# Kernel optimization log

Hardware: AMD Instinct MI355X
Metric: run time of the kernel (lower is better)

The kernel has to match this reference:

```python
import jax, jax.numpy as jnp
import numpy as np

N = 8192       # nodes
F_IN = 512     # input features
H = 8          # heads (layer 1)
C1 = 8         # per-head channels (layer 1)
NC = 16        # num classes
E = 262144     # edges (avg degree 32)
NEG_SLOPE = 0.2


def setup_inputs() -> dict:
    key = jax.random.key(0)
    ks = jax.random.split(key, 11)
    s = 0.1
    return {
        "x": jax.random.normal(ks[0], (N, F_IN), jnp.float32),
        "edge_index": jax.random.randint(ks[1], (2, E), 0, N, dtype=jnp.int32),
        "W1": jax.random.normal(ks[2], (F_IN, H * C1), jnp.float32) * s,
        "a_src1": jax.random.normal(ks[3], (H, C1), jnp.float32) * s,
        "a_dst1": jax.random.normal(ks[4], (H, C1), jnp.float32) * s,
        "b1": jnp.zeros((H * C1,), jnp.float32),
        "W2": jax.random.normal(ks[5], (H * C1, NC), jnp.float32) * s,
        "a_src2": jax.random.normal(ks[6], (1, NC), jnp.float32) * s,
        "a_dst2": jax.random.normal(ks[7], (1, NC), jnp.float32) * s,
        "b2": jnp.zeros((NC,), jnp.float32),
    }


def _gat_layer(x, W, a_src, a_dst, b, src, dst, heads, outc, concat):
    n = x.shape[0]
    h = (x @ W).reshape(n, heads, outc)                      # [N,H,C]
    al_s = jnp.einsum('nhc,hc->nh', h, a_src)                 # [N,H]
    al_d = jnp.einsum('nhc,hc->nh', h, a_dst)                 # [N,H]
    e = jax.nn.leaky_relu(al_s[src] + al_d[dst], NEG_SLOPE)   # [E,H]
    # segment softmax over destination node (every node has a self-loop)
    m = jax.ops.segment_max(e, dst, num_segments=n)
    ex = jnp.exp(e - m[dst])
    denom = jax.ops.segment_sum(ex, dst, num_segments=n)
    alpha = ex / denom[dst]                                   # [E,H]
    out = jax.ops.segment_sum(alpha[:, :, None] * h[src], dst, num_segments=n)  # [N,H,C]
    out = out.reshape(n, heads * outc) if concat else out.mean(axis=1)
    return out + b


def reference(x, edge_index, W1, a_src1, a_dst1, b1, W2, a_src2, a_dst2, b2):
    # add self-loops (PyG GATConv default)
    loop = jnp.arange(N, dtype=edge_index.dtype)
    src = jnp.concatenate([edge_index[0], loop])
    dst = jnp.concatenate([edge_index[1], loop])
    # dropout layers are identity in eval mode
    h1 = jax.nn.elu(_gat_layer(x, W1, a_src1, a_dst1, b1, src, dst, H, C1, True))
    z = _gat_layer(h1, W2, a_src2, a_dst2, b2, src, dst, 1, NC, False)
    return jax.nn.log_softmax(z, axis=-1), z @ z.T
```

## Files before the change

### kernel.cpp

```cpp
#include <hip/hip_runtime.h>
#include <math.h>

#define N_NODES 8192
#define F_IN 512
#define NH1 8
#define C1 8
#define D1 64
#define NC 16
#define E_EDGES 262144
#define TOT_EDGES (E_EDGES + N_NODES)
#define NEG_SLOPE 0.2f

__global__ __launch_bounds__(256) void gemm1_k(const float* __restrict__ x,
                                               const float* __restrict__ W1,
                                               float* __restrict__ h1pre) {
    __shared__ __align__(16) float As[32 * 68];
    __shared__ __align__(16) float Bs[32 * 68];
    int tid = threadIdx.x;
    int rowBase = blockIdx.x * 64;
    int rm = tid >> 4, rn = tid & 15;
    float acc[4][4] = {};
    for (int k0 = 0; k0 < F_IN; k0 += 32) {
#pragma unroll
        for (int j = 0; j < 8; ++j) {
            int i = tid + 256 * j;
            int r = i >> 5, c = i & 31;
            As[c * 68 + r] = x[(rowBase + r) * F_IN + k0 + c];
        }
#pragma unroll
        for (int j = 0; j < 8; ++j) {
            int i = tid + 256 * j;
            int rr = i >> 6, cc = i & 63;
            Bs[rr * 68 + cc] = W1[(k0 + rr) * D1 + cc];
        }
        __syncthreads();
#pragma unroll
        for (int kk = 0; kk < 32; ++kk) {
            float4 a = *(const float4*)&As[kk * 68 + rm * 4];
            float4 b = *(const float4*)&Bs[kk * 68 + rn * 4];
            float av[4] = {a.x, a.y, a.z, a.w};
            float bv[4] = {b.x, b.y, b.z, b.w};
#pragma unroll
            for (int jj = 0; jj < 4; ++jj)
#pragma unroll
                for (int ll = 0; ll < 4; ++ll)
                    acc[jj][ll] = fmaf(av[jj], bv[ll], acc[jj][ll]);
        }
        __syncthreads();
    }
#pragma unroll
    for (int jj = 0; jj < 4; ++jj) {
        float4 o = {acc[jj][0], acc[jj][1], acc[jj][2], acc[jj][3]};
        *(float4*)&h1pre[(size_t)(rowBase + rm * 4 + jj) * D1 + rn * 4] = o;
    }
}

__global__ void logits1_k(const float* __restrict__ h1pre,
                          const float* __restrict__ a_src1, const float* __restrict__ a_dst1,
                          float* __restrict__ als1, float* __restrict__ ald1) {
    int i = blockIdx.x * blockDim.x + threadIdx.x;
    if (i >= N_NODES * NH1) return;
    int h = i & 7;
    const float* hp = h1pre + (size_t)(i >> 3) * D1 + h * C1;
    float s = 0.f, d = 0.f;
#pragma unroll
    for (int c = 0; c < C1; ++c) {
        float v = hp[c];
        s = fmaf(v, a_src1[h * C1 + c], s);
        d = fmaf(v, a_dst1[h * C1 + c], d);
    }
    als1[i] = s;
    ald1[i] = d;
}

__global__ void hist_k(const int* __restrict__ ei, int* __restrict__ counts) {
    int i = blockIdx.x * blockDim.x + threadIdx.x;
    if (i >= TOT_EDGES) return;
    int dst = (i < E_EDGES) ? ei[E_EDGES + i] : (i - E_EDGES);
    atomicAdd(&counts[dst], 1);
}

__global__ __launch_bounds__(1024) void scan_k(const int* __restrict__ counts,
                                               int* __restrict__ offsets, int* __restrict__ cursor) {
    __shared__ int part[1024];
    int t = threadIdx.x;
    int local[8];
    int s = 0;
#pragma unroll
    for (int j = 0; j < 8; ++j) { local[j] = counts[t * 8 + j]; s += local[j]; }
    part[t] = s;
    __syncthreads();
    for (int d = 1; d < 1024; d <<= 1) {
        int v = (t >= d) ? part[t - d] : 0;
        __syncthreads();
        part[t] += v;
        __syncthreads();
    }
    int run = (t == 0) ? 0 : part[t - 1];
#pragma unroll
    for (int j = 0; j < 8; ++j) {
        offsets[t * 8 + j] = run;
        cursor[t * 8 + j] = run;
        run += local[j];
    }
    if (t == 1023) offsets[8192] = run;
}

__global__ void scatter_k(const int* __restrict__ ei, int* __restrict__ cursor, int* __restrict__ csr) {
    int i = blockIdx.x * blockDim.x + threadIdx.x;
    if (i >= TOT_EDGES) return;
    int src, dst;
    if (i < E_EDGES) { src = ei[i]; dst = ei[E_EDGES + i]; }
    else             { src = i - E_EDGES; dst = src; }
    int pos = atomicAdd(&cursor[dst], 1);
    csr[pos] = src;
}

__global__ __launch_bounds__(64) void agg1_k(const float* __restrict__ h1pre,
                                             const float* __restrict__ als1, const float* __restrict__ ald1,
                                             const int* __restrict__ offsets, const int* __restrict__ csr,
                                             const float* __restrict__ b1, float* __restrict__ out1) {
    int n = blockIdx.x, t = threadIdx.x;
    int beg = offsets[n], end = offsets[n + 1];
    int h = t & 7;
    float aldh = ald1[n * NH1 + h];
    float m = -3.4e38f;
    for (int i = beg + (t >> 3); i < end; i += 8) {
        int s = csr[i];
        float v = als1[s * NH1 + h] + aldh;
        v = v > 0.f ? v : NEG_SLOPE * v;
        m = fmaxf(m, v);
    }
    m = fmaxf(m, __shfl_xor(m, 8));
    m = fmaxf(m, __shfl_xor(m, 16));
    m = fmaxf(m, __shfl_xor(m, 32));
    float den = 0.f;
    for (int i = beg + (t >> 3); i < end; i += 8) {
        int s = csr[i];
        float v = als1[s * NH1 + h] + aldh;
        v = v > 0.f ? v : NEG_SLOPE * v;
        den += expf(v - m);
    }
    den += __shfl_xor(den, 8);
    den += __shfl_xor(den, 16);
    den += __shfl_xor(den, 32);
    int q = t >> 3;
    float mq = __shfl(m, q);
    float dq = __shfl(den, q);
    float aldq = ald1[n * NH1 + q];
    float acc = 0.f;
    for (int i = beg; i < end; ++i) {
        int s = csr[i];
        float v = als1[s * NH1 + q] + aldq;
        v = v > 0.f ? v : NEG_SLOPE * v;
        float w = expf(v - mq);
        acc = fmaf(w, h1pre[(size_t)s * D1 + t], acc);
    }
    float val = acc / dq + b1[t];
    out1[(size_t)n * D1 + t] = val > 0.f ? val : expm1f(val);
}

__global__ __launch_bounds__(256) void gemm2_k(const float* __restrict__ out1,
                                               const float* __restrict__ W2,
                                               float* __restrict__ h2pre) {
    __shared__ float w2s[D1 * NC];
    __shared__ float ot[16 * D1];
    int tid = threadIdx.x;
    int nb = blockIdx.x * 16;
#pragma unroll
    for (int j = 0; j < 4; ++j) {
        w2s[tid + 256 * j] = W2[tid + 256 * j];
        ot[tid + 256 * j] = out1[(size_t)nb * D1 + tid + 256 * j];
    }
    __syncthreads();
    int nl = tid >> 4, c = tid & 15;
    float acc = 0.f;
#pragma unroll
    for (int k = 0; k < D1; ++k) acc = fmaf(ot[nl * D1 + k], w2s[k * NC + c], acc);
    h2pre[(size_t)(nb + nl) * NC + c] = acc;
}

__global__ void logits2_k(const float* __restrict__ h2pre,
                          const float* __restrict__ a_src2, const float* __restrict__ a_dst2,
                          float* __restrict__ als2, float* __restrict__ ald2) {
    int n = blockIdx.x * blockDim.x + threadIdx.x;
    if (n >= N_NODES) return;
    const float* hp = h2pre + (size_t)n * NC;
    float s = 0.f, d = 0.f;
#pragma unroll
    for (int c = 0; c < NC; ++c) {
        float v = hp[c];
        s = fmaf(v, a_src2[c], s);
        d = fmaf(v, a_dst2[c], d);
    }
    als2[n] = s;
    ald2[n] = d;
}

__global__ __launch_bounds__(64) void agg2_k(const float* __restrict__ h2pre,
                                             const float* __restrict__ als2, const float* __restrict__ ald2,
                                             const int* __restrict__ offsets, const int* __restrict__ csr,
                                             const float* __restrict__ b2,
                                             float* __restrict__ z, float* __restrict__ out_ls) {
    int n = blockIdx.x, t = threadIdx.x;
    int beg = offsets[n], end = offsets[n + 1];
    float aldn = ald2[n];
    float m = -3.4e38f;
    for (int i = beg + t; i < end; i += 64) {
        float v = als2[csr[i]] + aldn;
        v = v > 0.f ? v : NEG_SLOPE * v;
        m = fmaxf(m, v);
    }
#pragma unroll
    for (int d = 1; d < 64; d <<= 1) m = fmaxf(m, __shfl_xor(m, d));
    float den = 0.f;
    for (int i = beg + t; i < end; i += 64) {
        float v = als2[csr[i]] + aldn;
        v = v > 0.f ? v : NEG_SLOPE * v;
        den += expf(v - m);
    }
#pragma unroll
    for (int d = 1; d < 64; d <<= 1) den += __shfl_xor(den, d);
    int eg = t >> 4, c = t & 15;
    float acc = 0.f;
    for (int i = beg + eg; i < end; i += 4) {
        int s = csr[i];
        float v = als2[s] + aldn;
        v = v > 0.f ? v : NEG_SLOPE * v;
        acc = fmaf(expf(v - m), h2pre[(size_t)s * NC + c], acc);
    }
    acc += __shfl_xor(acc, 16);
    acc += __shfl_xor(acc, 32);
    float zv = acc / den + b2[c];
    if (t < 16) z[(size_t)n * NC + t] = zv;
    float zm = zv;
#pragma unroll
    for (int d = 1; d < 16; d <<= 1) zm = fmaxf(zm, __shfl_xor(zm, d));
    float se = expf(zv - zm);
#pragma unroll
    for (int d = 1; d < 16; d <<= 1) se += __shfl_xor(se, d);
    if (t < 16) out_ls[(size_t)n * NC + t] = zv - (zm + logf(se));
}

__global__ __launch_bounds__(256) void gram_k(const float* __restrict__ z,
                                              float* __restrict__ out) {
    __shared__ __align__(16) float rz[64 * 16];
    int tid = threadIdx.x;
    int colBase = blockIdx.x * 256;
    int rowBase = blockIdx.y * 64;
    ((float4*)rz)[tid] = ((const float4*)z)[rowBase * 4 + tid];
    int j = colBase + tid;
    float c[16];
#pragma unroll
    for (int k4 = 0; k4 < 4; ++k4) {
        float4 v = ((const float4*)(z + (size_t)j * 16))[k4];
        c[k4 * 4 + 0] = v.x; c[k4 * 4 + 1] = v.y; c[k4 * 4 + 2] = v.z; c[k4 * 4 + 3] = v.w;
    }
    __syncthreads();
#pragma unroll 4
    for (int r = 0; r < 64; ++r) {
        const float* zr = &rz[r * 16];
        float acc = 0.f;
#pragma unroll
        for (int k = 0; k < 16; ++k) acc = fmaf(c[k], zr[k], acc);
        out[(size_t)(rowBase + r) * N_NODES + j] = acc;
    }
}

extern "C" void kernel_launch(void* const* d_in, const int* in_sizes, int n_in,
                              void* d_out, int out_size, void* d_ws, size_t ws_size,
                              hipStream_t stream) {
    (void)in_sizes; (void)n_in; (void)out_size; (void)ws_size;
    const float* x      = (const float*)d_in[0];
    const int*   ei     = (const int*)d_in[1];
    const float* W1     = (const float*)d_in[2];
    const float* a_src1 = (const float*)d_in[3];
    const float* a_dst1 = (const float*)d_in[4];
    const float* b1     = (const float*)d_in[5];
    const float* W2     = (const float*)d_in[6];
    const float* a_src2 = (const float*)d_in[7];
    const float* a_dst2 = (const float*)d_in[8];
    const float* b2     = (const float*)d_in[9];
    float* out = (float*)d_out;

    char* ws = (char*)d_ws;
    float* h1pre  = (float*)(ws + 0);
    float* out1   = (float*)(ws + 2097152);
    float* als1   = (float*)(ws + 4194304);
    float* ald1   = (float*)(ws + 4456448);
    float* h2pre  = (float*)(ws + 4718592);
    float* als2   = (float*)(ws + 5242880);
    float* ald2   = (float*)(ws + 5275648);
    float* zarr   = (float*)(ws + 5308416);
    int*   counts = (int*)  (ws + 5832704);
    int*   offsets= (int*)  (ws + 5865472);
    int*   cursor = (int*)  (ws + 5898496);
    int*   csr    = (int*)  (ws + 5931264);

    hipMemsetAsync(counts, 0, N_NODES * sizeof(int), stream);
    hist_k<<<(TOT_EDGES + 255) / 256, 256, 0, stream>>>(ei, counts);
    scan_k<<<1, 1024, 0, stream>>>(counts, offsets, cursor);
    scatter_k<<<(TOT_EDGES + 255) / 256, 256, 0, stream>>>(ei, cursor, csr);

    gemm1_k<<<N_NODES / 64, 256, 0, stream>>>(x, W1, h1pre);
    logits1_k<<<(N_NODES * NH1 + 255) / 256, 256, 0, stream>>>(h1pre, a_src1, a_dst1, als1, ald1);
    agg1_k<<<N_NODES, 64, 0, stream>>>(h1pre, als1, ald1, offsets, csr, b1, out1);

    gemm2_k<<<N_NODES / 16, 256, 0, stream>>>(out1, W2, h2pre);
    logits2_k<<<N_NODES / 256, 256, 0, stream>>>(h2pre, a_src2, a_dst2, als2, ald2);
    agg2_k<<<N_NODES, 64, 0, stream>>>(h2pre, als2, ald2, offsets, csr, b2, zarr, out);

    gram_k<<<dim3(N_NODES / 256, N_NODES / 64), 256, 0, stream>>>(zarr, out + (size_t)N_NODES * NC);
}
```

Before: 402.8 us.

## Use online softmax in aggregation, fuse logits2 into gemm2, nontemporal gram stores

Both aggregation kernels replace the three-pass segment softmax (max, denominator, weighted sum) with a single-pass online softmax, so the CSR and attention-logit gathers happen once instead of three times. Layer-2 partial states are merged across edge groups with shuffles. Each block now holds four nodes (256 threads), the logits2 kernel is folded into gemm2 through shared memory, and the large gram output uses nontemporal stores. The cost is two exps per edge instead of one in the hot loop, plus a serial dependency chain through the running max.

```diff
diff --git a/kernel.cpp b/kernel.cpp
--- a/kernel.cpp
+++ b/kernel.cpp
@@ -116,55 +116,41 @@
     csr[pos] = src;
 }
 
-__global__ __launch_bounds__(64) void agg1_k(const float* __restrict__ h1pre,
-                                             const float* __restrict__ als1, const float* __restrict__ ald1,
-                                             const int* __restrict__ offsets, const int* __restrict__ csr,
-                                             const float* __restrict__ b1, float* __restrict__ out1) {
-    int n = blockIdx.x, t = threadIdx.x;
+__global__ __launch_bounds__(256) void agg1_k(const float* __restrict__ h1pre,
+                                              const float* __restrict__ als1, const float* __restrict__ ald1,
+                                              const int* __restrict__ offsets, const int* __restrict__ csr,
+                                              const float* __restrict__ b1, float* __restrict__ out1) {
+    int n = blockIdx.x * 4 + (threadIdx.x >> 6);
+    int t = threadIdx.x & 63;
+    int q = t >> 3;
     int beg = offsets[n], end = offsets[n + 1];
-    int h = t & 7;
-    float aldh = ald1[n * NH1 + h];
-    float m = -3.4e38f;
-    for (int i = beg + (t >> 3); i < end; i += 8) {
-        int s = csr[i];
-        float v = als1[s * NH1 + h] + aldh;
-        v = v > 0.f ? v : NEG_SLOPE * v;
-        m = fmaxf(m, v);
-    }
-    m = fmaxf(m, __shfl_xor(m, 8));
-    m = fmaxf(m, __shfl_xor(m, 16));
-    m = fmaxf(m, __shfl_xor(m, 32));
-    float den = 0.f;
-    for (int i = beg + (t >> 3); i < end; i += 8) {
-        int s = csr[i];
-        float v = als1[s * NH1 + h] + aldh;
-        v = v > 0.f ? v : NEG_SLOPE * v;
-        den += expf(v - m);
-    }
-    den += __shfl_xor(den, 8);
-    den += __shfl_xor(den, 16);
-    den += __shfl_xor(den, 32);
-    int q = t >> 3;
-    float mq = __shfl(m, q);
-    float dq = __shfl(den, q);
     float aldq = ald1[n * NH1 + q];
-    float acc = 0.f;
+    float m = -3.4e38f, den = 0.f, acc = 0.f;
     for (int i = beg; i < end; ++i) {
         int s = csr[i];
         float v = als1[s * NH1 + q] + aldq;
         v = v > 0.f ? v : NEG_SLOPE * v;
-        float w = expf(v - mq);
-        acc = fmaf(w, h1pre[(size_t)s * D1 + t], acc);
-    }
-    float val = acc / dq + b1[t];
+        float hv = h1pre[(size_t)s * D1 + t];
+        float nm = fmaxf(m, v);
+        float alpha = expf(m - nm);
+        float w = expf(v - nm);
+        den = den * alpha + w;
+        acc = fmaf(acc, alpha, w * hv);
+        m = nm;
+    }
+    float val = acc / den + b1[t];
     out1[(size_t)n * D1 + t] = val > 0.f ? val : expm1f(val);
 }
 
 __global__ __launch_bounds__(256) void gemm2_k(const float* __restrict__ out1,
                                                const float* __restrict__ W2,
-                                               float* __restrict__ h2pre) {
+                                               const float* __restrict__ a_src2,
+                                               const float* __restrict__ a_dst2,
+                                               float* __restrict__ h2pre,
+                                               float* __restrict__ als2, float* __restrict__ ald2) {
     __shared__ float w2s[D1 * NC];
     __shared__ float ot[16 * D1];
+    __shared__ float h2s[16 * NC];
     int tid = threadIdx.x;
     int nb = blockIdx.x * 16;
 #pragma unroll
@@ -178,68 +164,64 @@
 #pragma unroll
     for (int k = 0; k < D1; ++k) acc = fmaf(ot[nl * D1 + k], w2s[k * NC + c], acc);
     h2pre[(size_t)(nb + nl) * NC + c] = acc;
-}
-
-__global__ void logits2_k(const float* __restrict__ h2pre,
-                          const float* __restrict__ a_src2, const float* __restrict__ a_dst2,
-                          float* __restrict__ als2, float* __restrict__ ald2) {
-    int n = blockIdx.x * blockDim.x + threadIdx.x;
-    if (n >= N_NODES) return;
-    const float* hp = h2pre + (size_t)n * NC;
-    float s = 0.f, d = 0.f;
-#pragma unroll
-    for (int c = 0; c < NC; ++c) {
-        float v = hp[c];
-        s = fmaf(v, a_src2[c], s);
-        d = fmaf(v, a_dst2[c], d);
-    }
-    als2[n] = s;
-    ald2[n] = d;
-}
-
-__global__ __launch_bounds__(64) void agg2_k(const float* __restrict__ h2pre,
-                                             const float* __restrict__ als2, const float* __restrict__ ald2,
-                                             const int* __restrict__ offsets, const int* __restrict__ csr,
-                                             const float* __restrict__ b2,
-                                             float* __restrict__ z, float* __restrict__ out_ls) {
-    int n = blockIdx.x, t = threadIdx.x;
+    h2s[nl * NC + c] = acc;
+    __syncthreads();
+    if (tid < 16) {
+        float s = 0.f, d = 0.f;
+#pragma unroll
+        for (int k = 0; k < NC; ++k) {
+            float v = h2s[tid * NC + k];
+            s = fmaf(v, a_src2[k], s);
+            d = fmaf(v, a_dst2[k], d);
+        }
+        als2[nb + tid] = s;
+        ald2[nb + tid] = d;
+    }
+}
+
+__global__ __launch_bounds__(256) void agg2_k(const float* __restrict__ h2pre,
+                                              const float* __restrict__ als2, const float* __restrict__ ald2,
+                                              const int* __restrict__ offsets, const int* __restrict__ csr,
+                                              const float* __restrict__ b2,
+                                              float* __restrict__ z, float* __restrict__ out_ls) {
+    int n = blockIdx.x * 4 + (threadIdx.x >> 6);
+    int t = threadIdx.x & 63;
     int beg = offsets[n], end = offsets[n + 1];
     float aldn = ald2[n];
-    float m = -3.4e38f;
-    for (int i = beg + t; i < end; i += 64) {
-        float v = als2[csr[i]] + aldn;
-        v = v > 0.f ? v : NEG_SLOPE * v;
-        m = fmaxf(m, v);
-    }
-#pragma unroll
-    for (int d = 1; d < 64; d <<= 1) m = fmaxf(m, __shfl_xor(m, d));
-    float den = 0.f;
-    for (int i = beg + t; i < end; i += 64) {
-        float v = als2[csr[i]] + aldn;
-        v = v > 0.f ? v : NEG_SLOPE * v;
-        den += expf(v - m);
-    }
-#pragma unroll
-    for (int d = 1; d < 64; d <<= 1) den += __shfl_xor(den, d);
     int eg = t >> 4, c = t & 15;
-    float acc = 0.f;
+    float m = -3.4e38f, den = 0.f, acc = 0.f;
     for (int i = beg + eg; i < end; i += 4) {
         int s = csr[i];
         float v = als2[s] + aldn;
         v = v > 0.f ? v : NEG_SLOPE * v;
-        acc = fmaf(expf(v - m), h2pre[(size_t)s * NC + c], acc);
-    }
-    acc += __shfl_xor(acc, 16);
-    acc += __shfl_xor(acc, 32);
+        float hv = h2pre[(size_t)s * NC + c];
+        float nm = fmaxf(m, v);
+        float alpha = expf(m - nm);
+        float w = expf(v - nm);
+        den = den * alpha + w;
+        acc = fmaf(acc, alpha, w * hv);
+        m = nm;
+    }
+#pragma unroll
+    for (int d = 16; d < 64; d <<= 1) {
+        float mo = __shfl_xor(m, d), dno = __shfl_xor(den, d), aco = __shfl_xor(acc, d);
+        float nm = fmaxf(m, mo);
+        float a1 = expf(m - nm), a2 = expf(mo - nm);
+        den = den * a1 + dno * a2;
+        acc = acc * a1 + aco * a2;
+        m = nm;
+    }
     float zv = acc / den + b2[c];
-    if (t < 16) z[(size_t)n * NC + t] = zv;
     float zm = zv;
 #pragma unroll
     for (int d = 1; d < 16; d <<= 1) zm = fmaxf(zm, __shfl_xor(zm, d));
     float se = expf(zv - zm);
 #pragma unroll
     for (int d = 1; d < 16; d <<= 1) se += __shfl_xor(se, d);
-    if (t < 16) out_ls[(size_t)n * NC + t] = zv - (zm + logf(se));
+    if (t < 16) {
+        z[(size_t)n * NC + t] = zv;
+        out_ls[(size_t)n * NC + t] = zv - (zm + logf(se));
+    }
 }
 
 __global__ __launch_bounds__(256) void gram_k(const float* __restrict__ z,
@@ -263,7 +245,7 @@
         float acc = 0.f;
 #pragma unroll
         for (int k = 0; k < 16; ++k) acc = fmaf(c[k], zr[k], acc);
-        out[(size_t)(rowBase + r) * N_NODES + j] = acc;
+        __builtin_nontemporal_store(acc, &out[(size_t)(rowBase + r) * N_NODES + j]);
     }
 }
 
@@ -304,11 +286,10 @@
 
     gemm1_k<<<N_NODES / 64, 256, 0, stream>>>(x, W1, h1pre);
     logits1_k<<<(N_NODES * NH1 + 255) / 256, 256, 0, stream>>>(h1pre, a_src1, a_dst1, als1, ald1);
-    agg1_k<<<N_NODES, 64, 0, stream>>>(h1pre, als1, ald1, offsets, csr, b1, out1);
-
-    gemm2_k<<<N_NODES / 16, 256, 0, stream>>>(out1, W2, h2pre);
-    logits2_k<<<N_NODES / 256, 256, 0, stream>>>(h2pre, a_src2, a_dst2, als2, ald2);
-    agg2_k<<<N_NODES, 64, 0, stream>>>(h2pre, als2, ald2, offsets, csr, b2, zarr, out);
+    agg1_k<<<N_NODES / 4, 256, 0, stream>>>(h1pre, als1, ald1, offsets, csr, b1, out1);
+
+    gemm2_k<<<N_NODES / 16, 256, 0, stream>>>(out1, W2, a_src2, a_dst2, h2pre, als2, ald2);
+    agg2_k<<<N_NODES / 4, 256, 0, stream>>>(h2pre, als2, ald2, offsets, csr, b2, zarr, out);
 
     gram_k<<<dim3(N_NODES / 256, N_NODES / 64), 256, 0, stream>>>(zarr, out + (size_t)N_NODES * NC);
 }
```

After: 407.1 us. About the same (+1.1%).
